# Optimization experiments

Hardware: AMD Instinct MI355X
Metric: run time of the kernel (lower is better)

The kernel has to match this reference:

```python
import jax, jax.numpy as jnp
import numpy as np

B, BOND, N, ATOM, UNITS = 256, 5, 128, 64, 128


def setup_inputs() -> dict:
    key = jax.random.key(0)
    k1, k2, k3 = jax.random.split(key, 3)
    adjacency = jax.random.uniform(k1, (B, BOND, N, N), dtype=jnp.float32)
    features = jax.random.normal(k2, (B, N, ATOM), dtype=jnp.float32)
    # per-sample unique kernel: (global_batch, bond_dim, atom_dim, units)
    kernel = jax.random.normal(k3, (B, BOND, ATOM, UNITS), dtype=jnp.float32) * 0.05
    return {"adjacency": adjacency, "features": features, "kernel": kernel}


def reference(adjacency, features, kernel):
    # aggregate neighbors per bond type: [B, bond, N, atom]
    x = jnp.einsum('bemn,bnd->bemd', adjacency, features)
    # per-sample, per-bond linear transform: [B, bond, N, units]
    x = jnp.einsum('bemd,bedu->bemu', x, kernel)
    # reduce over bond types, then activation: [B, N, units]
    return jax.nn.relu(jnp.sum(x, axis=1))
```

## Files before the change

kernel.cpp:

```cpp
#include <hip/hip_runtime.h>


typedef __attribute__((ext_vector_type(8))) short s8v;
typedef __attribute__((ext_vector_type(4))) float f4v;

__device__ __forceinline__ short f2bf(float f) {
    unsigned u = __builtin_bit_cast(unsigned, f);
    u += 0x7FFFu + ((u >> 16) & 1u);
    return (short)(u >> 16);
}

__global__ __launch_bounds__(512, 2)
void rgc_kernel(const float* __restrict__ adj,
                const float* __restrict__ feat,
                const float* __restrict__ ker,
                float* __restrict__ out)
{
    __shared__ __align__(16) short featT[64][136];
    __shared__ __align__(16) short kerT[2][128][72];
    __shared__ __align__(16) short YB[128][72];

    const int b    = blockIdx.x;
    const int tid  = threadIdx.x;
    const int w    = tid >> 6;
    const int lane = tid & 63;
    const int c16  = lane & 15;
    const int quad = lane >> 4;

    const float* adjB  = adj  + (size_t)b * (5 * 128 * 128);
    const float* featB = feat + (size_t)b * (128 * 64);
    const float* kerB  = ker  + (size_t)b * (5 * 64 * 128);
    float*       outB  = out  + (size_t)b * (128 * 128);

    {
        f4v fv[4];
        #pragma unroll
        for (int i = 0; i < 4; ++i)
            fv[i] = *(const f4v*)(featB + (i * 512 + tid) * 4);
        #pragma unroll
        for (int i = 0; i < 4; ++i) {
            int g = i * 512 + tid;
            int n = g >> 4, d0 = (g & 15) << 2;
            #pragma unroll
            for (int j = 0; j < 4; ++j)
                featT[d0 + j][n] = f2bf(fv[i][j]);
        }
    }
    {
        f4v kv[4];
        #pragma unroll
        for (int i = 0; i < 4; ++i)
            kv[i] = *(const f4v*)(kerB + (i * 512 + tid) * 4);
        #pragma unroll
        for (int i = 0; i < 4; ++i) {
            int g = i * 512 + tid;
            int d = g >> 5, u0 = (g & 31) << 2;
            #pragma unroll
            for (int j = 0; j < 4; ++j)
                kerT[0][u0 + j][d] = f2bf(kv[i][j]);
        }
    }
    __syncthreads();

    f4v oacc[8] = {};

    for (int e = 0; e < 5; ++e) {
        const float* ap = adjB + e * (128 * 128) + (16 * w + c16) * 128 + 8 * quad;
        f4v a0[4], a1[4];
        #pragma unroll
        for (int k16 = 0; k16 < 4; ++k16) {
            a0[k16] = *(const f4v*)(ap + 32 * k16);
            a1[k16] = *(const f4v*)(ap + 32 * k16 + 4);
        }
        f4v kv[4];
        const int en = e + 1;
        if (en < 5) {
            #pragma unroll
            for (int i = 0; i < 4; ++i)
                kv[i] = *(const f4v*)(kerB + en * (64 * 128) + (i * 512 + tid) * 4);
        }

        f4v yacc[4] = {};
        #pragma unroll
        for (int k16 = 0; k16 < 4; ++k16) {
            s8v af;
            #pragma unroll
            for (int j = 0; j < 4; ++j) af[j] = f2bf(a0[k16][j]);
            #pragma unroll
            for (int j = 0; j < 4; ++j) af[4 + j] = f2bf(a1[k16][j]);
            #pragma unroll
            for (int d16 = 0; d16 < 4; ++d16) {
                s8v bf = *(const s8v*)&featT[16 * d16 + c16][32 * k16 + 8 * quad];
                yacc[d16] = __builtin_amdgcn_mfma_f32_16x16x32_bf16(af, bf, yacc[d16], 0, 0, 0);
            }
        }

        #pragma unroll
        for (int d16 = 0; d16 < 4; ++d16)
            #pragma unroll
            for (int r = 0; r < 4; ++r)
                YB[16 * w + 4 * quad + r][16 * d16 + c16] = f2bf(yacc[d16][r]);

        if (en < 5) {
            #pragma unroll
            for (int i = 0; i < 4; ++i) {
                int g = i * 512 + tid;
                int d = g >> 5, u0 = (g & 31) << 2;
                #pragma unroll
                for (int j = 0; j < 4; ++j)
                    kerT[en & 1][u0 + j][d] = f2bf(kv[i][j]);
            }
        }

        {
            const int buf = e & 1;
            s8v afr0 = *(const s8v*)&YB[16 * w + c16][8 * quad];
            s8v afr1 = *(const s8v*)&YB[16 * w + c16][32 + 8 * quad];
            #pragma unroll
            for (int u16 = 0; u16 < 8; ++u16) {
                s8v b0 = *(const s8v*)&kerT[buf][16 * u16 + c16][8 * quad];
                s8v b1 = *(const s8v*)&kerT[buf][16 * u16 + c16][32 + 8 * quad];
                oacc[u16] = __builtin_amdgcn_mfma_f32_16x16x32_bf16(afr0, b0, oacc[u16], 0, 0, 0);
                oacc[u16] = __builtin_amdgcn_mfma_f32_16x16x32_bf16(afr1, b1, oacc[u16], 0, 0, 0);
            }
        }
        __syncthreads();
    }

    #pragma unroll
    for (int u16 = 0; u16 < 8; ++u16)
        #pragma unroll
        for (int r = 0; r < 4; ++r)
            outB[(16 * w + 4 * quad + r) * 128 + 16 * u16 + c16] = fmaxf(oacc[u16][r], 0.f);
}

extern "C" void kernel_launch(void* const* d_in, const int* in_sizes, int n_in,
                              void* d_out, int out_size, void* d_ws, size_t ws_size,
                              hipStream_t stream)
{
    const float* adj  = (const float*)d_in[0];
    const float* feat = (const float*)d_in[1];
    const float* ker  = (const float*)d_in[2];
    rgc_kernel<<<256, 512, 0, stream>>>(adj, feat, ker, (float*)d_out);
}
```

Measured before the change: 170.1 us.

## Split work across 1024 threads, prefetch adjacency, use fragment-native LDS layout

Doubles the block to 1024 threads, with wave pairs sharing a 16-row tile. Each wave in a pair computes the full aggregation but only half of the output units. Shared-memory tiles are stored in MFMA-fragment order so each lane does one contiguous 16-byte read, which removes the transposed strided LDS accesses. Adjacency for the next bond is now prefetched a stage ahead, and the loop drops its final barrier. The cost is that the first-stage aggregation MFMAs and adjacency loads are duplicated across each wave pair, and register pressure rises under the 1024-thread launch bound.

```diff
diff --git a/kernel.cpp b/kernel.cpp
--- a/kernel.cpp
+++ b/kernel.cpp
@@ -10,128 +10,140 @@
     return (short)(u >> 16);
 }
 
-__global__ __launch_bounds__(512, 2)
+__global__ __launch_bounds__(1024, 4)
 void rgc_kernel(const float* __restrict__ adj,
                 const float* __restrict__ feat,
                 const float* __restrict__ ker,
                 float* __restrict__ out)
 {
-    __shared__ __align__(16) short featT[64][136];
-    __shared__ __align__(16) short kerT[2][128][72];
-    __shared__ __align__(16) short YB[128][72];
+    __shared__ __align__(16) short featB[16 * 512];
+    __shared__ __align__(16) short kerB[2][16 * 512];
+    __shared__ __align__(16) short YA[16][2 * 512];
 
-    const int b    = blockIdx.x;
     const int tid  = threadIdx.x;
     const int w    = tid >> 6;
     const int lane = tid & 63;
     const int c16  = lane & 15;
     const int quad = lane >> 4;
+    const int g    = w >> 1;
+    const int h    = w & 1;
 
-    const float* adjB  = adj  + (size_t)b * (5 * 128 * 128);
-    const float* featB = feat + (size_t)b * (128 * 64);
-    const float* kerB  = ker  + (size_t)b * (5 * 64 * 128);
-    float*       outB  = out  + (size_t)b * (128 * 128);
+    const int b = blockIdx.x;
+    const float* adjB = adj  + (size_t)b * (5 * 128 * 128);
+    const float* feG  = feat + (size_t)b * (128 * 64);
+    const float* keG  = ker  + (size_t)b * (5 * 64 * 128);
+    float*       outB = out  + (size_t)b * (128 * 128);
 
+    f4v a0[4], a1[4];
     {
-        f4v fv[4];
-        #pragma unroll
-        for (int i = 0; i < 4; ++i)
-            fv[i] = *(const f4v*)(featB + (i * 512 + tid) * 4);
-        #pragma unroll
-        for (int i = 0; i < 4; ++i) {
-            int g = i * 512 + tid;
-            int n = g >> 4, d0 = (g & 15) << 2;
-            #pragma unroll
-            for (int j = 0; j < 4; ++j)
-                featT[d0 + j][n] = f2bf(fv[i][j]);
-        }
-    }
-    {
-        f4v kv[4];
-        #pragma unroll
-        for (int i = 0; i < 4; ++i)
-            kv[i] = *(const f4v*)(kerB + (i * 512 + tid) * 4);
-        #pragma unroll
-        for (int i = 0; i < 4; ++i) {
-            int g = i * 512 + tid;
-            int d = g >> 5, u0 = (g & 31) << 2;
-            #pragma unroll
-            for (int j = 0; j < 4; ++j)
-                kerT[0][u0 + j][d] = f2bf(kv[i][j]);
-        }
-    }
-    __syncthreads();
-
-    f4v oacc[8] = {};
-
-    for (int e = 0; e < 5; ++e) {
-        const float* ap = adjB + e * (128 * 128) + (16 * w + c16) * 128 + 8 * quad;
-        f4v a0[4], a1[4];
+        const float* ap = adjB + (16 * g + c16) * 128 + 8 * quad;
         #pragma unroll
         for (int k16 = 0; k16 < 4; ++k16) {
             a0[k16] = *(const f4v*)(ap + 32 * k16);
             a1[k16] = *(const f4v*)(ap + 32 * k16 + 4);
         }
-        f4v kv[4];
-        const int en = e + 1;
-        if (en < 5) {
+    }
+
+    {
+        const int fd  = tid & 63;
+        const int fn0 = (tid >> 6) * 8;
+        float fv[8];
+        #pragma unroll
+        for (int j = 0; j < 8; ++j)
+            fv[j] = feG[(fn0 + j) * 64 + fd];
+        s8v v;
+        #pragma unroll
+        for (int j = 0; j < 8; ++j) v[j] = f2bf(fv[j]);
+        *(s8v*)&featB[((fd >> 4) * 4 + (fn0 >> 5)) * 512 + ((fn0 >> 3) & 3) * 128 + (fd & 15) * 8] = v;
+    }
+
+    const int ku  = tid & 127;
+    const int kd0 = (tid >> 7) * 8;
+    const int kerB_off = (ku >> 4) * 1024 + (kd0 >> 5) * 512 + ((kd0 >> 3) & 3) * 128 + (ku & 15) * 8;
+    {
+        float kv[8];
+        #pragma unroll
+        for (int j = 0; j < 8; ++j)
+            kv[j] = keG[(kd0 + j) * 128 + ku];
+        s8v v;
+        #pragma unroll
+        for (int j = 0; j < 8; ++j) v[j] = f2bf(kv[j]);
+        *(s8v*)&kerB[0][kerB_off] = v;
+    }
+    __syncthreads();
+
+    f4v oacc[4] = {};
+
+    for (int e = 0; e < 5; ++e) {
+        s8v af[4];
+        #pragma unroll
+        for (int k16 = 0; k16 < 4; ++k16) {
             #pragma unroll
-            for (int i = 0; i < 4; ++i)
-                kv[i] = *(const f4v*)(kerB + en * (64 * 128) + (i * 512 + tid) * 4);
+            for (int j = 0; j < 4; ++j) {
+                af[k16][j]     = f2bf(a0[k16][j]);
+                af[k16][4 + j] = f2bf(a1[k16][j]);
+            }
+        }
+
+        float kv[8];
+        if (e < 4) {
+            const float* kp = keG + (e + 1) * (64 * 128);
+            #pragma unroll
+            for (int j = 0; j < 8; ++j)
+                kv[j] = kp[(kd0 + j) * 128 + ku];
+            const float* ap = adjB + (e + 1) * (128 * 128) + (16 * g + c16) * 128 + 8 * quad;
+            #pragma unroll
+            for (int k16 = 0; k16 < 4; ++k16) {
+                a0[k16] = *(const f4v*)(ap + 32 * k16);
+                a1[k16] = *(const f4v*)(ap + 32 * k16 + 4);
+            }
         }
 
         f4v yacc[4] = {};
         #pragma unroll
-        for (int k16 = 0; k16 < 4; ++k16) {
-            s8v af;
-            #pragma unroll
-            for (int j = 0; j < 4; ++j) af[j] = f2bf(a0[k16][j]);
-            #pragma unroll
-            for (int j = 0; j < 4; ++j) af[4 + j] = f2bf(a1[k16][j]);
+        for (int k16 = 0; k16 < 4; ++k16)
             #pragma unroll
             for (int d16 = 0; d16 < 4; ++d16) {
-                s8v bf = *(const s8v*)&featT[16 * d16 + c16][32 * k16 + 8 * quad];
-                yacc[d16] = __builtin_amdgcn_mfma_f32_16x16x32_bf16(af, bf, yacc[d16], 0, 0, 0);
+                s8v bf = *(const s8v*)&featB[(d16 * 4 + k16) * 512 + lane * 8];
+                yacc[d16] = __builtin_amdgcn_mfma_f32_16x16x32_bf16(af[k16], bf, yacc[d16], 0, 0, 0);
             }
-        }
 
         #pragma unroll
-        for (int d16 = 0; d16 < 4; ++d16)
+        for (int d16 = 0; d16 < 4; ++d16) {
+            const int base = (d16 >> 1) * 512 + ((2 * d16 + (c16 >> 3)) & 3) * 128 + (c16 & 7);
             #pragma unroll
             for (int r = 0; r < 4; ++r)
-                YB[16 * w + 4 * quad + r][16 * d16 + c16] = f2bf(yacc[d16][r]);
-
-        if (en < 5) {
-            #pragma unroll
-            for (int i = 0; i < 4; ++i) {
-                int g = i * 512 + tid;
-                int d = g >> 5, u0 = (g & 31) << 2;
-                #pragma unroll
-                for (int j = 0; j < 4; ++j)
-                    kerT[en & 1][u0 + j][d] = f2bf(kv[i][j]);
-            }
+                YA[w][base + (4 * quad + r) * 8] = f2bf(yacc[d16][r]);
         }
 
         {
             const int buf = e & 1;
-            s8v afr0 = *(const s8v*)&YB[16 * w + c16][8 * quad];
-            s8v afr1 = *(const s8v*)&YB[16 * w + c16][32 + 8 * quad];
+            s8v afr0 = *(const s8v*)&YA[w][lane * 8];
+            s8v afr1 = *(const s8v*)&YA[w][512 + lane * 8];
             #pragma unroll
-            for (int u16 = 0; u16 < 8; ++u16) {
-                s8v b0 = *(const s8v*)&kerT[buf][16 * u16 + c16][8 * quad];
-                s8v b1 = *(const s8v*)&kerT[buf][16 * u16 + c16][32 + 8 * quad];
-                oacc[u16] = __builtin_amdgcn_mfma_f32_16x16x32_bf16(afr0, b0, oacc[u16], 0, 0, 0);
-                oacc[u16] = __builtin_amdgcn_mfma_f32_16x16x32_bf16(afr1, b1, oacc[u16], 0, 0, 0);
+            for (int n = 0; n < 4; ++n) {
+                const int u16 = 4 * h + n;
+                s8v b0 = *(const s8v*)&kerB[buf][(u16 * 2 + 0) * 512 + lane * 8];
+                s8v b1 = *(const s8v*)&kerB[buf][(u16 * 2 + 1) * 512 + lane * 8];
+                oacc[n] = __builtin_amdgcn_mfma_f32_16x16x32_bf16(afr0, b0, oacc[n], 0, 0, 0);
+                oacc[n] = __builtin_amdgcn_mfma_f32_16x16x32_bf16(afr1, b1, oacc[n], 0, 0, 0);
             }
         }
-        __syncthreads();
+
+        if (e < 4) {
+            s8v v;
+            #pragma unroll
+            for (int j = 0; j < 8; ++j) v[j] = f2bf(kv[j]);
+            *(s8v*)&kerB[(e + 1) & 1][kerB_off] = v;
+            __syncthreads();
+        }
     }
 
     #pragma unroll
-    for (int u16 = 0; u16 < 8; ++u16)
+    for (int n = 0; n < 4; ++n)
         #pragma unroll
         for (int r = 0; r < 4; ++r)
-            outB[(16 * w + 4 * quad + r) * 128 + 16 * u16 + c16] = fmaxf(oacc[u16][r], 0.f);
+            outB[(16 * g + 4 * quad + r) * 128 + 16 * (4 * h + n) + c16] = fmaxf(oacc[n][r], 0.f);
 }
 
 extern "C" void kernel_launch(void* const* d_in, const int* in_sizes, int n_in,
@@ -141,5 +153,5 @@
     const float* adj  = (const float*)d_in[0];
     const float* feat = (const float*)d_in[1];
     const float* ker  = (const float*)d_in[2];
-    rgc_kernel<<<256, 512, 0, stream>>>(adj, feat, ker, (float*)d_out);
+    rgc_kernel<<<256, 1024, 0, stream>>>(adj, feat, ker, (float*)d_out);
 }
```

After: 171.6 us. About the same (+0.9%).
